# Kernel optimization log

Hardware: AMD Instinct MI355X
Metric: run time of the kernel (lower is better)

Reference implementation:

```python
import jax, jax.numpy as jnp
import numpy as np

N = 100000   # n_entity
D = 128      # kg_emb_dim
R = 12       # n_relation
NB = 8       # num_bases
E = 1_000_000
P = 400_000  # hypergraph incidences
HE = 20_000  # hyperedges
B = 64       # users in batch
LR = 64      # related entities per hypergraph per user
LC = 32      # context entities per user
NH = 8       # mha heads
HD = D // NH


def setup_inputs() -> dict:
    key = jax.random.key(0)
    ks = jax.random.split(key, 32)
    s = 1.0 / np.sqrt(D)
    f = lambda i, shape, sc=s: jax.random.normal(ks[i], shape, dtype=jnp.float32) * sc
    ri = lambda i, shape, hi: jax.random.randint(ks[i], shape, 0, hi, dtype=jnp.int32)
    return {
        'entity_emb': f(0, (N, D)),
        'rgcn_bases': f(1, (NB, D, D)),
        'rgcn_comp': f(2, (R, NB)),
        'rgcn_root': f(3, (D, D)),
        'rgcn_bias': jnp.zeros((D,), jnp.float32),
        'sess_theta': f(4, (D, D)),
        'sess_bias': jnp.zeros((D,), jnp.float32),
        'know_theta': f(5, (D, D)),
        'know_bias': jnp.zeros((D,), jnp.float32),
        'in_proj_w': f(6, (3 * D, D)),
        'in_proj_b': jnp.zeros((3 * D,), jnp.float32),
        'out_proj_w': f(7, (D, D)),
        'out_proj_b': jnp.zeros((D,), jnp.float32),
        'attn_his_a': f(8, (D, D)),
        'attn_his_b': f(9, (D, 1)),
        'attn_a': f(10, (D, D)),
        'attn_b': f(11, (D, 1)),
        'rec_bias': jnp.zeros((N,), jnp.float32),
        'edge_src': ri(12, (E,), N),
        'edge_dst': ri(13, (E,), N),
        'edge_type': ri(14, (E,), R),
        'sess_nodes': ri(15, (P,), N),
        'sess_edges': ri(16, (P,), HE),
        'know_nodes': ri(17, (P,), N),
        'know_edges': ri(18, (P,), HE),
        'sess_rel_idx': ri(19, (B, LR), N),
        'know_rel_idx': ri(20, (B, LR), N),
        'context_idx': ri(21, (B, LC), N),
    }


def rgcn_conv(x, bases, comp, root, bias, src, dst, etype):
    # PyG RGCNConv with basis decomposition; per-relation mean aggregation
    # norm = 1/|N_r(i)| : count edges per (dst, relation)
    pair_key = dst * R + etype
    cnt = jax.ops.segment_sum(jnp.ones_like(src, dtype=x.dtype), pair_key, N * R)
    norm = 1.0 / jnp.maximum(cnt[pair_key], 1.0)  # [E]
    w = jnp.einsum('rb,bio->rio', comp, bases)    # [R, D, D]
    out = x @ root + bias
    for r in range(R):
        h_r = x @ w[r]                                            # [N, D]
        coef = norm * (etype == r).astype(x.dtype)                # [E]
        out = out + jax.ops.segment_sum(h_r[src] * coef[:, None], dst, N)
    return out


def hypergraph_conv(x, theta, bias, nodes, edges, n_hyperedges):
    # PyG HypergraphConv (no attention): D^-1 H W B^-1 H^T X Theta + bias
    xt = x @ theta                                                # [N, D]
    ones = jnp.ones(nodes.shape, x.dtype)
    b_deg = jax.ops.segment_sum(ones, edges, n_hyperedges)        # [HE]
    edge_feat = jax.ops.segment_sum(xt[nodes], edges, n_hyperedges)
    edge_feat = edge_feat * jnp.where(b_deg > 0, 1.0 / b_deg, 0.0)[:, None]
    d_deg = jax.ops.segment_sum(ones, nodes, N)                   # [N]
    out = jax.ops.segment_sum(edge_feat[edges], nodes, N)
    return out * jnp.where(d_deg > 0, 1.0 / d_deg, 0.0)[:, None] + bias


def self_attn_batch(h, a, b):
    # SelfAttentionBatch: e = tanh(h a) b; softmax over nodes; weighted sum
    e = jnp.einsum('bld,dk->blk', jnp.tanh(jnp.einsum('bld,de->ble', h, a)), b)[..., 0]
    attn = jax.nn.softmax(e, axis=-1)                             # [B, L]
    return jnp.einsum('bl,bld->bd', attn, h)


def mha(q, kv, in_proj_w, in_proj_b, out_proj_w, out_proj_b):
    # torch.nn.MultiheadAttention (batch_first) math
    wq, wk, wv = in_proj_w[:D], in_proj_w[D:2 * D], in_proj_w[2 * D:]
    bq, bk, bv = in_proj_b[:D], in_proj_b[D:2 * D], in_proj_b[2 * D:]
    qh = (q @ wq.T + bq).reshape(q.shape[0], q.shape[1], NH, HD)
    kh = (kv @ wk.T + bk).reshape(kv.shape[0], kv.shape[1], NH, HD)
    vh = (kv @ wv.T + bv).reshape(kv.shape[0], kv.shape[1], NH, HD)
    logits = jnp.einsum('bqhd,bkhd->bhqk', qh, kh) / np.sqrt(HD)
    attn = jax.nn.softmax(logits, axis=-1)
    o = jnp.einsum('bhqk,bkhd->bqhd', attn, vh).reshape(q.shape[0], q.shape[1], D)
    return o @ out_proj_w.T + out_proj_b


def reference(entity_emb, rgcn_bases, rgcn_comp, rgcn_root, rgcn_bias,
              sess_theta, sess_bias, know_theta, know_bias,
              in_proj_w, in_proj_b, out_proj_w, out_proj_b,
              attn_his_a, attn_his_b, attn_a, attn_b, rec_bias,
              edge_src, edge_dst, edge_type,
              sess_nodes, sess_edges, know_nodes, know_edges,
              sess_rel_idx, know_rel_idx, context_idx):
    # 1) RGCN over the full KG
    kg = rgcn_conv(entity_emb, rgcn_bases, rgcn_comp, rgcn_root, rgcn_bias,
                   edge_src, edge_dst, edge_type)
    # 2) session / knowledge hypergraph convolutions on RGCN output
    sess = hypergraph_conv(kg, sess_theta, sess_bias, sess_nodes, sess_edges, HE)
    know = hypergraph_conv(kg, know_theta, know_bias, know_nodes, know_edges, HE)
    # 3) per-user: related = concat(session_emb, knowledge_emb); context from kg
    related = jnp.concatenate([sess[sess_rel_idx], know[know_rel_idx]], axis=1)  # [B, 2LR, D]
    context = kg[context_idx]                                                    # [B, LC, D]
    # 4) MHItemAttention (context queries related) + gated attention pooling
    att_rel = mha(context, related, in_proj_w, in_proj_b, out_proj_w, out_proj_b)
    his = self_attn_batch(att_rel, attn_his_a, attn_his_b)                       # [B, D]
    user_cat = jnp.concatenate([context, his[:, None, :]], axis=1)               # [B, LC+1, D]
    user = self_attn_batch(user_cat, attn_a, attn_b)                             # [B, D]
    # 5) recommendation scores: F.linear(user, kg_embedding, rec_bias.bias)
    return user @ kg.T + rec_bias                                                # [B, N]
```

## Files before the change

### kernel.cpp

```cpp
#include <hip/hip_runtime.h>
#include <hip/hip_bf16.h>

#define DN 100000
#define DD 128
#define DR 12
#define DNB 8
#define DE 1000000
#define DP 400000
#define DHE 20000
#define DHE2 40000
#define DB 64
#define DLR 64
#define DLC 32
#define DNH 8
#define DHD 16
#define NRBINS (DR * DN)
#define NALLBINS (NRBINS + DHE2)
#define SCAN_CHUNK 1024
#define MCAP 65536

typedef unsigned short ushortT;
typedef unsigned int uintT;
typedef __attribute__((ext_vector_type(8))) short s8v;
typedef __attribute__((ext_vector_type(4))) float f4v;

#define APAD 136
#define ASLB 40

__device__ __forceinline__ ushortT rneb(float v) {
    uintT b = __float_as_uint(v);
    return (ushortT)((b + 0x7FFFu + ((b >> 16) & 1u)) >> 16);
}
__device__ __forceinline__ float b2f(ushortT h) {
    return __uint_as_float(((uintT)h) << 16);
}

__device__ __forceinline__ void split_store8(ushortT* hbase, ushortT* lbase, const float* v)
{
    ushortT h[8], l[8];
    #pragma unroll
    for (int j = 0; j < 8; ++j) {
        h[j] = rneb(v[j]);
        l[j] = rneb(v[j] - b2f(h[j]));
    }
    uint4 hv = make_uint4((uintT)h[0] | ((uintT)h[1] << 16), (uintT)h[2] | ((uintT)h[3] << 16),
                          (uintT)h[4] | ((uintT)h[5] << 16), (uintT)h[6] | ((uintT)h[7] << 16));
    uint4 lv = make_uint4((uintT)l[0] | ((uintT)l[1] << 16), (uintT)l[2] | ((uintT)l[3] << 16),
                          (uintT)l[4] | ((uintT)l[5] << 16), (uintT)l[6] | ((uintT)l[7] << 16));
    *(uint4*)hbase = hv;
    *(uint4*)lbase = lv;
}

__global__ __launch_bounds__(256) void k_presplit_all(
    const float* __restrict__ root, const float* __restrict__ st,
    const float* __restrict__ kt, const float* __restrict__ ipw,
    const float* __restrict__ opw, const float* __restrict__ aha,
    const float* __restrict__ aa, ushortT* __restrict__ outA)
{
    int gid = blockIdx.x * 256 + threadIdx.x;
    int mat = gid >> 14, e = gid & 16383;
    const float* srcs[9] = {root, st, kt, ipw, ipw + 16384, ipw + 32768, opw, aha, aa};
    const float* W = srcs[mat];
    bool t1 = (mat >= 3 && mat <= 6);
    int k = e & 31, n = (e >> 5) & 127, kc = e >> 12;
    float f = t1 ? W[(size_t)n * 128 + kc * 32 + k] : W[(size_t)(kc * 32 + k) * 128 + n];
    ushortT h = rneb(f);
    outA[(size_t)mat * 32768 + e] = h;
    outA[(size_t)mat * 32768 + 16384 + e] = rneb(f - b2f(h));
}

__global__ void k_wcomp_split(const float* __restrict__ comp, const float* __restrict__ bases,
                              ushortT* __restrict__ warena)
{
    int i = blockIdx.x * blockDim.x + threadIdx.x;
    if (i >= DR * DD * DD) return;
    int r = i / (DD * DD), io = i % (DD * DD);
    float s = 0.f;
    #pragma unroll
    for (int b = 0; b < DNB; ++b) s += comp[r * DNB + b] * bases[(size_t)b * DD * DD + io];
    int irow = io >> 7, o = io & 127;
    int kc = irow >> 5, k = irow & 31;
    size_t dst = (size_t)r * 32768 + (size_t)kc * 4096 + o * 32 + k;
    ushortT h = rneb(s);
    warena[dst] = h;
    warena[dst + 16384] = rneb(s - b2f(h));
}

__global__ __launch_bounds__(256) void k_gemm_ds(
    const float* __restrict__ A, const ushortT* __restrict__ Wb,
    const float* __restrict__ bias, const float* __restrict__ rs,
    const int* __restrict__ gidx, float* __restrict__ gout,
    float* __restrict__ C, int M)
{
    __shared__ __align__(16) ushortT Ah[64 * APAD], Al[64 * APAD];
    __shared__ __align__(16) ushortT Bs[8192];
    int tid = threadIdx.x;
    int row0 = blockIdx.x * 64;
    {
        int row = tid >> 2, c0 = (tid & 3) * 32;
        int gr = row0 + row;
        int arow = gr;
        if (gidx && gr < M) arow = gidx[gr];
        const float* ar = A + (size_t)arow * 128 + c0;
        float sc = 1.0f;
        if (rs && gr < M) { float d = rs[gr]; sc = (d > 0.f) ? 1.0f / d : 0.f; }
        #pragma unroll
        for (int g = 0; g < 4; ++g) {
            float v[8] = {};
            if (gr < M) {
                float4 u0 = *(const float4*)(ar + g * 8);
                float4 u1 = *(const float4*)(ar + g * 8 + 4);
                v[0]=u0.x*sc; v[1]=u0.y*sc; v[2]=u0.z*sc; v[3]=u0.w*sc;
                v[4]=u1.x*sc; v[5]=u1.y*sc; v[6]=u1.z*sc; v[7]=u1.w*sc;
                if (gout) {
                    *(float4*)(gout + (size_t)gr * 128 + c0 + g * 8)     = u0;
                    *(float4*)(gout + (size_t)gr * 128 + c0 + g * 8 + 4) = u1;
                }
            }
            split_store8(&Ah[row * APAD + c0 + g * 8], &Al[row * APAD + c0 + g * 8], v);
        }
    }
    f4v acc[8] = {};
    int w = tid >> 6, lane = tid & 63, m = lane & 15, quad = lane >> 4;
    for (int kc = 0; kc < 4; ++kc) {
        __syncthreads();
        {
            const ushortT* gh = Wb + kc * 4096;
            const ushortT* gl = Wb + 16384 + kc * 4096;
            *(s8v*)&Bs[tid * 8]        = *(const s8v*)&gh[tid * 8];
            *(s8v*)&Bs[2048 + tid * 8] = *(const s8v*)&gh[2048 + tid * 8];
            *(s8v*)&Bs[4096 + tid * 8] = *(const s8v*)&gl[tid * 8];
            *(s8v*)&Bs[6144 + tid * 8] = *(const s8v*)&gl[2048 + tid * 8];
        }
        __syncthreads();
        s8v ah = *(const s8v*)&Ah[(w * 16 + m) * APAD + kc * 32 + quad * 8];
        s8v al = *(const s8v*)&Al[(w * 16 + m) * APAD + kc * 32 + quad * 8];
        #pragma unroll
        for (int nt = 0; nt < 8; ++nt) {
            int boff = (nt * 16 + m) * 32 + quad * 8;
            s8v bh = *(const s8v*)&Bs[boff];
            s8v bl = *(const s8v*)&Bs[4096 + boff];
            acc[nt] = __builtin_amdgcn_mfma_f32_16x16x32_bf16(ah, bh, acc[nt], 0, 0, 0);
            acc[nt] = __builtin_amdgcn_mfma_f32_16x16x32_bf16(al, bh, acc[nt], 0, 0, 0);
            acc[nt] = __builtin_amdgcn_mfma_f32_16x16x32_bf16(ah, bl, acc[nt], 0, 0, 0);
        }
    }
    float bv[8];
    #pragma unroll
    for (int nt = 0; nt < 8; ++nt) bv[nt] = bias ? bias[nt * 16 + m] : 0.f;
    #pragma unroll
    for (int rr = 0; rr < 4; ++rr) {
        int gr = row0 + w * 16 + quad * 4 + rr;
        if (gr < M) {
            #pragma unroll
            for (int nt = 0; nt < 8; ++nt)
                C[(size_t)gr * 128 + nt * 16 + m] = acc[nt][rr] + bv[nt];
        }
    }
}

__global__ __launch_bounds__(256) void k_tanh_dot_ds(
    const float* __restrict__ A, const ushortT* __restrict__ Wb,
    const float* __restrict__ bvec, float* __restrict__ e, int M)
{
    __shared__ __align__(16) ushortT Ah[64 * APAD], Al[64 * APAD];
    __shared__ __align__(16) ushortT Bs[8192];
    int tid = threadIdx.x;
    int row0 = blockIdx.x * 64;
    {
        int row = tid >> 2, c0 = (tid & 3) * 32;
        int gr = row0 + row;
        const float* ar = A + (size_t)gr * 128 + c0;
        #pragma unroll
        for (int g = 0; g < 4; ++g) {
            float v[8] = {};
            if (gr < M) {
                float4 u0 = *(const float4*)(ar + g * 8);
                float4 u1 = *(const float4*)(ar + g * 8 + 4);
                v[0]=u0.x; v[1]=u0.y; v[2]=u0.z; v[3]=u0.w;
                v[4]=u1.x; v[5]=u1.y; v[6]=u1.z; v[7]=u1.w;
            }
            split_store8(&Ah[row * APAD + c0 + g * 8], &Al[row * APAD + c0 + g * 8], v);
        }
    }
    f4v acc[8] = {};
    int w = tid >> 6, lane = tid & 63, m = lane & 15, quad = lane >> 4;
    for (int kc = 0; kc < 4; ++kc) {
        __syncthreads();
        {
            const ushortT* gh = Wb + kc * 4096;
            const ushortT* gl = Wb + 16384 + kc * 4096;
            *(s8v*)&Bs[tid * 8]        = *(const s8v*)&gh[tid * 8];
            *(s8v*)&Bs[2048 + tid * 8] = *(const s8v*)&gh[2048 + tid * 8];
            *(s8v*)&Bs[4096 + tid * 8] = *(const s8v*)&gl[tid * 8];
            *(s8v*)&Bs[6144 + tid * 8] = *(const s8v*)&gl[2048 + tid * 8];
        }
        __syncthreads();
        s8v ah = *(const s8v*)&Ah[(w * 16 + m) * APAD + kc * 32 + quad * 8];
        s8v al = *(const s8v*)&Al[(w * 16 + m) * APAD + kc * 32 + quad * 8];
        #pragma unroll
        for (int nt = 0; nt < 8; ++nt) {
            int boff = (nt * 16 + m) * 32 + quad * 8;
            s8v bh = *(const s8v*)&Bs[boff];
            s8v bl = *(const s8v*)&Bs[4096 + boff];
            acc[nt] = __builtin_amdgcn_mfma_f32_16x16x32_bf16(ah, bh, acc[nt], 0, 0, 0);
            acc[nt] = __builtin_amdgcn_mfma_f32_16x16x32_bf16(al, bh, acc[nt], 0, 0, 0);
            acc[nt] = __builtin_amdgcn_mfma_f32_16x16x32_bf16(ah, bl, acc[nt], 0, 0, 0);
        }
    }
    float bv[8];
    #pragma unroll
    for (int nt = 0; nt < 8; ++nt) bv[nt] = bvec[nt * 16 + m];
    #pragma unroll
    for (int rr = 0; rr < 4; ++rr) {
        float p = 0.f;
        #pragma unroll
        for (int nt = 0; nt < 8; ++nt) p += tanhf(acc[nt][rr]) * bv[nt];
        #pragma unroll
        for (int o = 1; o < 16; o <<= 1) p += __shfl_xor(p, o);
        int gr = row0 + w * 16 + quad * 4 + rr;
        if (m == 0 && gr < M) e[gr] = p;
    }
}

template <int L>
__global__ __launch_bounds__(128) void k_pool_apply(const float* __restrict__ h,
                                                    const float* __restrict__ e,
                                                    float* __restrict__ out,
                                                    ushortT* __restrict__ us)
{
    __shared__ float es[L];
    int b = blockIdx.x, tid = threadIdx.x;
    if (tid < L) es[tid] = e[b * L + tid];
    __syncthreads();
    float mx = -1e30f;
    #pragma unroll
    for (int l = 0; l < L; ++l) mx = fmaxf(mx, es[l]);
    float wgt[L];
    float sum = 0.f;
    #pragma unroll
    for (int l = 0; l < L; ++l) { wgt[l] = __expf(es[l] - mx); sum += wgt[l]; }
    float inv = 1.0f / sum;
    float o = 0.f;
    #pragma unroll
    for (int l = 0; l < L; ++l) o += wgt[l] * h[((size_t)b * L + l) * 128 + tid];
    float val = o * inv;
    out[(size_t)b * 128 + tid] = val;
    if (us) {
        ushortT hh = rneb(val);
        ushortT ll = rneb(val - b2f(hh));
        int e_ = ((tid >> 5) * 2048) + b * 32 + (tid & 31);
        us[e_] = hh;
        us[8192 + e_] = ll;
    }
}

__global__ void k_build_ucat(const float* __restrict__ ctx, const float* __restrict__ his,
                             float* ucat)
{
    int i = blockIdx.x * blockDim.x + threadIdx.x;
    if (i >= DB * 33 * 128) return;
    int d = i & 127, l = (i >> 7) % 33, b = i / (33 * 128);
    ucat[i] = (l < 32) ? ctx[((size_t)b * 32 + l) * 128 + d] : his[(size_t)b * 128 + d];
}

__global__ __launch_bounds__(256) void k_rgcn_fk(
    const float* __restrict__ x, const ushortT* __restrict__ rootsplit,
    const ushortT* __restrict__ warena, const float* __restrict__ bias,
    const int* __restrict__ soff, const int* __restrict__ hist,
    const int* __restrict__ ssrc, float* __restrict__ kg)
{
    __shared__ __align__(16) ushortT Ah[64 * ASLB], Al[64 * ASLB];
    __shared__ __align__(16) ushortT Bs[8192];
    int tid = threadIdx.x;
    int dst0 = blockIdx.x * 64;
    int nrow = min(64, DN - dst0);
    int w = tid >> 6, lane = tid & 63, m = lane & 15, quad = lane >> 4;
    int row = tid >> 2, ci = (tid & 3) * 8;
    f4v acc[8] = {};

    for (int s = 0; s < 52; ++s) {
        int r = (s - 4) >> 2, kci = (s - 4) & 3;
        __syncthreads();
        {
            float a[8] = {};
            if (row < nrow) {
                if (s < 4) {
                    const float* ar = x + (size_t)(dst0 + row) * 128 + s * 32 + ci;
                    float4 u0 = *(const float4*)ar, u1 = *(const float4*)(ar + 4);
                    a[0]=u0.x; a[1]=u0.y; a[2]=u0.z; a[3]=u0.w;
                    a[4]=u1.x; a[5]=u1.y; a[6]=u1.z; a[7]=u1.w;
                } else {
                    int key = (dst0 + row) * DR + r;
                    int len = hist[key];
                    int st = soff[key] - len;
                    int cb = kci * 32 + ci;
                    for (int i = 0; i < len; ++i) {
                        const float* xr = x + (size_t)ssrc[st + i] * 128 + cb;
                        float4 v0 = *(const float4*)xr, v1 = *(const float4*)(xr + 4);
                        a[0]+=v0.x; a[1]+=v0.y; a[2]+=v0.z; a[3]+=v0.w;
                        a[4]+=v1.x; a[5]+=v1.y; a[6]+=v1.z; a[7]+=v1.w;
                    }
                    float inv = (len > 0) ? 1.0f / (float)len : 0.f;
                    #pragma unroll
                    for (int j = 0; j < 8; ++j) a[j] *= inv;
                }
            }
            split_store8(&Ah[row * ASLB + ci], &Al[row * ASLB + ci], a);
        }
        {
            const ushortT* bb = (s < 4) ? rootsplit + s * 4096
                                        : warena + (size_t)r * 32768 + kci * 4096;
            const ushortT* bl = (s < 4) ? rootsplit + 16384 + s * 4096
                                        : warena + (size_t)r * 32768 + 16384 + kci * 4096;
            *(s8v*)&Bs[tid * 8]        = *(const s8v*)&bb[tid * 8];
            *(s8v*)&Bs[2048 + tid * 8] = *(const s8v*)&bb[2048 + tid * 8];
            *(s8v*)&Bs[4096 + tid * 8] = *(const s8v*)&bl[tid * 8];
            *(s8v*)&Bs[6144 + tid * 8] = *(const s8v*)&bl[2048 + tid * 8];
        }
        __syncthreads();
        s8v ah = *(const s8v*)&Ah[(w * 16 + m) * ASLB + quad * 8];
        s8v al = *(const s8v*)&Al[(w * 16 + m) * ASLB + quad * 8];
        #pragma unroll
        for (int nt = 0; nt < 8; ++nt) {
            int boff = (nt * 16 + m) * 32 + quad * 8;
            s8v bh = *(const s8v*)&Bs[boff];
            s8v bl2 = *(const s8v*)&Bs[4096 + boff];
            acc[nt] = __builtin_amdgcn_mfma_f32_16x16x32_bf16(ah, bh, acc[nt], 0, 0, 0);
            acc[nt] = __builtin_amdgcn_mfma_f32_16x16x32_bf16(al, bh, acc[nt], 0, 0, 0);
            acc[nt] = __builtin_amdgcn_mfma_f32_16x16x32_bf16(ah, bl2, acc[nt], 0, 0, 0);
        }
    }
    float bv[8];
    #pragma unroll
    for (int nt = 0; nt < 8; ++nt) bv[nt] = bias[nt * 16 + m];
    #pragma unroll
    for (int rr = 0; rr < 4; ++rr) {
        int gr = dst0 + w * 16 + quad * 4 + rr;
        if (gr < DN) {
            #pragma unroll
            for (int nt = 0; nt < 8; ++nt)
                kg[(size_t)gr * 128 + nt * 16 + m] = acc[nt][rr] + bv[nt];
        }
    }
}

__global__ __launch_bounds__(256) void k_score_ds(
    const float* __restrict__ kg, const ushortT* __restrict__ Ub,
    const float* __restrict__ rb, float* __restrict__ out)
{
    __shared__ __align__(16) ushortT Ah[64 * APAD], Al[64 * APAD];
    __shared__ __align__(16) ushortT Bs[4096];
    int tid = threadIdx.x;
    int n0 = blockIdx.x * 64;
    {
        int row = tid >> 2, c0 = (tid & 3) * 32;
        int gr = n0 + row;
        const float* ar = kg + (size_t)gr * 128 + c0;
        #pragma unroll
        for (int g = 0; g < 4; ++g) {
            float v[8] = {};
            if (gr < DN) {
                float4 u0 = *(const float4*)(ar + g * 8);
                float4 u1 = *(const float4*)(ar + g * 8 + 4);
                v[0]=u0.x; v[1]=u0.y; v[2]=u0.z; v[3]=u0.w;
                v[4]=u1.x; v[5]=u1.y; v[6]=u1.z; v[7]=u1.w;
            }
            split_store8(&Ah[row * APAD + c0 + g * 8], &Al[row * APAD + c0 + g * 8], v);
        }
    }
    f4v acc[4] = {};
    int w = tid >> 6, lane = tid & 63, m = lane & 15, quad = lane >> 4;
    for (int kc = 0; kc < 4; ++kc) {
        __syncthreads();
        {
            const ushortT* gh = Ub + kc * 2048;
            const ushortT* gl = Ub + 8192 + kc * 2048;
            *(s8v*)&Bs[tid * 8]        = *(const s8v*)&gh[tid * 8];
            *(s8v*)&Bs[2048 + tid * 8] = *(const s8v*)&gl[tid * 8];
        }
        __syncthreads();
        s8v ah = *(const s8v*)&Ah[(w * 16 + m) * APAD + kc * 32 + quad * 8];
        s8v al = *(const s8v*)&Al[(w * 16 + m) * APAD + kc * 32 + quad * 8];
        #pragma unroll
        for (int nt = 0; nt < 4; ++nt) {
            int boff = (nt * 16 + m) * 32 + quad * 8;
            s8v bh = *(const s8v*)&Bs[boff];
            s8v bl = *(const s8v*)&Bs[2048 + boff];
            acc[nt] = __builtin_amdgcn_mfma_f32_16x16x32_bf16(ah, bh, acc[nt], 0, 0, 0);
            acc[nt] = __builtin_amdgcn_mfma_f32_16x16x32_bf16(al, bh, acc[nt], 0, 0, 0);
            acc[nt] = __builtin_amdgcn_mfma_f32_16x16x32_bf16(ah, bl, acc[nt], 0, 0, 0);
        }
    }
    int n = n0 + w * 16 + quad * 4;
    if (n < DN) {
        float4 rbv = *(const float4*)&rb[n];
        #pragma unroll
        for (int nt = 0; nt < 4; ++nt) {
            int b = nt * 16 + m;
            float4 o = make_float4(acc[nt][0] + rbv.x, acc[nt][1] + rbv.y,
                                   acc[nt][2] + rbv.z, acc[nt][3] + rbv.w);
            *(float4*)&out[(size_t)b * DN + n] = o;
        }
    }
}

__global__ void k_scan_pass1(const int* __restrict__ in, int n, int* __restrict__ bsum)
{
    __shared__ int red[256];
    int b = blockIdx.x, t = threadIdx.x;
    int i0 = b * SCAN_CHUNK + t * 4;
    int s = 0;
    #pragma unroll
    for (int j = 0; j < 4; ++j) {
        int i = i0 + j;
        if (i < n) s += in[i];
    }
    red[t] = s;
    __syncthreads();
    for (int o = 128; o > 0; o >>= 1) {
        if (t < o) red[t] += red[t + o];
        __syncthreads();
    }
    if (t == 0) bsum[b] = red[0];
}

__global__ __launch_bounds__(256) void k_scan_pass2p(int* bsum, int nb, int* total)
{
    __shared__ int lds[256];
    __shared__ int carry;
    int t = threadIdx.x;
    if (t == 0) carry = 0;
    __syncthreads();
    for (int c0 = 0; c0 < nb; c0 += 256) {
        int i = c0 + t;
        int v = (i < nb) ? bsum[i] : 0;
        lds[t] = v;
        __syncthreads();
        for (int o = 1; o < 256; o <<= 1) {
            int add = (t >= o) ? lds[t - o] : 0;
            __syncthreads();
            lds[t] += add;
            __syncthreads();
        }
        int myc = carry;
        if (i < nb) bsum[i] = lds[t] - v + myc;
        int tot = lds[255];
        __syncthreads();
        if (t == 0) carry = myc + tot;
        __syncthreads();
    }
    if (total && t == 0) *total = carry;
}

__global__ void k_scan_pass3(const int* __restrict__ in, int n, const int* __restrict__ bsum,
                             int* __restrict__ out)
{
    __shared__ int lds[256];
    int b = blockIdx.x, t = threadIdx.x;
    int i0 = b * SCAN_CHUNK + t * 4;
    int v[4]; int s = 0;
    #pragma unroll
    for (int j = 0; j < 4; ++j) {
        int i = i0 + j;
        int x = 0;
        if (i < n) x = in[i];
        v[j] = x; s += x;
    }
    lds[t] = s;
    __syncthreads();
    for (int o = 1; o < 256; o <<= 1) {
        int add = (t >= o) ? lds[t - o] : 0;
        __syncthreads();
        lds[t] += add;
        __syncthreads();
    }
    int run = lds[t] - s + bsum[b];
    #pragma unroll
    for (int j = 0; j < 4; ++j) {
        int i = i0 + j;
        if (i < n) { out[i] = run; run += v[j]; }
    }
}

__global__ void k_hist_both(const int* __restrict__ dst, const int* __restrict__ et,
                            int* __restrict__ hist,
                            const int* __restrict__ se, const int* __restrict__ ke)
{
    int i = blockIdx.x * blockDim.x + threadIdx.x;
    if (i < DE) {
        atomicAdd(&hist[dst[i] * DR + et[i]], 1);
    } else {
        int j = i - DE;
        if (j < DP) atomicAdd(&hist[NRBINS + se[j]], 1);
        else if (j < 2 * DP) atomicAdd(&hist[NRBINS + DHE + ke[j - DP]], 1);
    }
}

__global__ void k_bucket_both(const int* __restrict__ src, const int* __restrict__ dst,
                              const int* __restrict__ et, int* __restrict__ soff,
                              int* __restrict__ ssrc,
                              const int* __restrict__ sn, const int* __restrict__ se,
                              const int* __restrict__ kn, const int* __restrict__ ke,
                              int* __restrict__ pns)
{
    int i = blockIdx.x * blockDim.x + threadIdx.x;
    if (i < DE) {
        int key = dst[i] * DR + et[i];
        int pos = atomicAdd(&soff[key], 1);
        ssrc[pos] = src[i];
    } else {
        int j = i - DE;
        if (j >= 2 * DP) return;
        int e, node;
        if (j < DP) { e = se[j]; node = sn[j]; }
        else { e = DHE + ke[j - DP]; node = kn[j - DP]; }
        int pos = atomicAdd(&soff[NRBINS + e], 1);
        pns[pos - DE] = node;
    }
}

__global__ void k_hyper_agg(const float* __restrict__ xsrc, const int* __restrict__ pns,
                            const int* __restrict__ hoff, const int* __restrict__ hcnt,
                            const int* __restrict__ heneed, float* __restrict__ efeat)
{
    int lane = threadIdx.x & 63;
    int he = (blockIdx.x * blockDim.x + threadIdx.x) >> 6;
    if (he >= DHE2) return;
    if (!heneed[he]) return;
    int len = hcnt[he];
    int st = hoff[he] - len - DE;
    int half = lane >> 5;
    int c16 = (lane & 31) * 4;
    float4 acc = make_float4(0.f, 0.f, 0.f, 0.f);
    int c = 0;
    for (; c + 4 <= len; c += 4) {
        int n0 = pns[st + c + half];
        int n1 = pns[st + c + 2 + half];
        float4 v0 = *(const float4*)&xsrc[(size_t)n0 * 128 + c16];
        float4 v1 = *(const float4*)&xsrc[(size_t)n1 * 128 + c16];
        acc.x += v0.x + v1.x; acc.y += v0.y + v1.y;
        acc.z += v0.z + v1.z; acc.w += v0.w + v1.w;
    }
    for (; c < len; c += 2) {
        int idx = c + half;
        if (idx < len) {
            int n = pns[st + idx];
            float4 v = *(const float4*)&xsrc[(size_t)n * 128 + c16];
            acc.x += v.x; acc.y += v.y; acc.z += v.z; acc.w += v.w;
        }
    }
    acc.x += __shfl_xor(acc.x, 32);
    acc.y += __shfl_xor(acc.y, 32);
    acc.z += __shfl_xor(acc.z, 32);
    acc.w += __shfl_xor(acc.w, 32);
    if (half == 0) {
        float inv = (len > 0) ? 1.0f / (float)len : 0.f;
        float4 o = make_float4(acc.x * inv, acc.y * inv, acc.z * inv, acc.w * inv);
        *(float4*)&efeat[(size_t)he * 128 + c16] = o;
    }
}

__global__ void k_slot_assign2(const int* __restrict__ sidx, const int* __restrict__ kidx,
                               int* slot_s, int* slot_k, int* scnt)
{
    int i = blockIdx.x * blockDim.x + threadIdx.x;
    if (i < DB * DLR) {
        int node = sidx[i];
        if (atomicCAS(&slot_s[node], -1, -2) == -1) slot_s[node] = atomicAdd(&scnt[0], 1);
    } else if (i < 2 * DB * DLR) {
        int node = kidx[i - DB * DLR];
        if (atomicCAS(&slot_k[node], -1, -2) == -1) slot_k[node] = atomicAdd(&scnt[1], 1);
    }
}

__global__ __launch_bounds__(256) void k_sdeg_match(
    const int* __restrict__ nodes, const int* __restrict__ he, const int* __restrict__ slot,
    float* sdeg, int* mcnt, int* mhe, int* msl, int* heneed, int heBase)
{
    __shared__ int lcnt, lbase;
    if (threadIdx.x == 0) lcnt = 0;
    __syncthreads();
    int i = blockIdx.x * 256 + threadIdx.x;
    int s = -1, lidx = 0, h = 0;
    if (i < DP) {
        s = slot[nodes[i]];
        if (s >= 0) {
            h = heBase + he[i];
            heneed[h] = 1;
            atomicAdd(&sdeg[s], 1.0f);
            lidx = atomicAdd(&lcnt, 1);
        }
    }
    __syncthreads();
    if (threadIdx.x == 0) lbase = (lcnt > 0) ? atomicAdd(mcnt, lcnt) : 0;
    __syncthreads();
    if (s >= 0) {
        int idx = lbase + lidx;
        if (idx < MCAP) { mhe[idx] = h; msl[idx] = s; }
    }
}

__global__ void k_accmatch2(const float* __restrict__ efeat,
                            const int* __restrict__ mhe_s, const int* __restrict__ msl_s,
                            const int* __restrict__ mhe_k, const int* __restrict__ msl_k,
                            const int* __restrict__ mcnt,
                            float* sacc_s, float* sacc_k)
{
    int lane = threadIdx.x & 63;
    int w = (blockIdx.x * blockDim.x + threadIdx.x) >> 6;
    int nw = (gridDim.x * blockDim.x) >> 6;
    int Ms = min(mcnt[0], MCAP), Mk = min(mcnt[1], MCAP);
    for (int i = w; i < Ms + Mk; i += nw) {
        bool sess = i < Ms;
        int he = sess ? mhe_s[i] : mhe_k[i - Ms];
        int sl = sess ? msl_s[i] : msl_k[i - Ms];
        float* sacc = sess ? sacc_s : sacc_k;
        float2 v = *(const float2*)&efeat[(size_t)he * 128 + lane * 2];
        atomicAdd(&sacc[(size_t)sl * 128 + lane * 2],     v.x);
        atomicAdd(&sacc[(size_t)sl * 128 + lane * 2 + 1], v.y);
    }
}

__global__ void k_rel_gather2(const float* __restrict__ so_s, const float* __restrict__ so_k,
                              const int* __restrict__ slot_s, const int* __restrict__ slot_k,
                              const int* __restrict__ ridx_s, const int* __restrict__ ridx_k,
                              float* __restrict__ related)
{
    int gid = blockIdx.x * blockDim.x + threadIdx.x;
    int i = gid >> 5, c = gid & 31;
    if (i >= 2 * DB * DLR) return;
    bool sess = i < DB * DLR;
    int ii = sess ? i : i - DB * DLR;
    int s = sess ? slot_s[ridx_s[ii]] : slot_k[ridx_k[ii]];
    const float* so = sess ? so_s : so_k;
    int b = ii / DLR, l = ii % DLR;
    int colOff = sess ? 0 : 64;
    ((float4*)&related[((size_t)b * 128 + colOff + l) * 128])[c] =
        ((const float4*)&so[(size_t)s * 128])[c];
}

__global__ __launch_bounds__(256) void k_mha(const float* __restrict__ qb,
                                             const float* __restrict__ kb,
                                             const float* __restrict__ vb,
                                             float* __restrict__ ob)
{
    int b = blockIdx.x >> 3, h = blockIdx.x & 7;
    __shared__ float Ks[128][16], Vs[128][16], Qs[32][16];
    int tid = threadIdx.x;
    for (int i = tid; i < 128 * 16; i += 256) {
        int j = i >> 4, d = i & 15;
        Ks[j][d] = kb[((size_t)b * 128 + j) * 128 + h * 16 + d];
        Vs[j][d] = vb[((size_t)b * 128 + j) * 128 + h * 16 + d];
    }
    for (int i = tid; i < 32 * 16; i += 256) {
        int q = i >> 4, d = i & 15;
        Qs[q][d] = qb[((size_t)b * 32 + q) * 128 + h * 16 + d] * 0.25f;
    }
    __syncthreads();
    int q = tid >> 3;
    int jg = tid & 7;
    float lg[16];
    float m = -1e30f;
    #pragma unroll
    for (int jj = 0; jj < 16; ++jj) {
        int j = jg * 16 + jj;
        float s = 0.f;
        #pragma unroll
        for (int d = 0; d < 16; ++d) s += Qs[q][d] * Ks[j][d];
        lg[jj] = s;
        m = fmaxf(m, s);
    }
    #pragma unroll
    for (int o = 1; o < 8; o <<= 1) m = fmaxf(m, __shfl_xor(m, o));
    float sum = 0.f;
    float acc[16] = {};
    #pragma unroll
    for (int jj = 0; jj < 16; ++jj) {
        float p = __expf(lg[jj] - m);
        sum += p;
        int j = jg * 16 + jj;
        #pragma unroll
        for (int d = 0; d < 16; ++d) acc[d] += p * Vs[j][d];
    }
    #pragma unroll
    for (int o = 1; o < 8; o <<= 1) {
        sum += __shfl_xor(sum, o);
        #pragma unroll
        for (int d = 0; d < 16; ++d) acc[d] += __shfl_xor(acc[d], o);
    }
    if (jg == 0) {
        float inv = 1.0f / sum;
        #pragma unroll
        for (int d = 0; d < 16; ++d)
            ob[((size_t)b * 32 + q) * 128 + h * 16 + d] = acc[d] * inv;
    }
}

extern "C" void kernel_launch(void* const* d_in, const int* in_sizes, int n_in,
                              void* d_out, int out_size, void* d_ws, size_t ws_size,
                              hipStream_t stream)
{
    const float* emb        = (const float*)d_in[0];
    const float* bases      = (const float*)d_in[1];
    const float* comp       = (const float*)d_in[2];
    const float* root       = (const float*)d_in[3];
    const float* rgcn_bias  = (const float*)d_in[4];
    const float* sess_theta = (const float*)d_in[5];
    const float* sess_bias  = (const float*)d_in[6];
    const float* know_theta = (const float*)d_in[7];
    const float* know_bias  = (const float*)d_in[8];
    const float* in_proj_w  = (const float*)d_in[9];
    const float* in_proj_b  = (const float*)d_in[10];
    const float* out_proj_w = (const float*)d_in[11];
    const float* out_proj_b = (const float*)d_in[12];
    const float* attn_his_a = (const float*)d_in[13];
    const float* attn_his_b = (const float*)d_in[14];
    const float* attn_a     = (const float*)d_in[15];
    const float* attn_b     = (const float*)d_in[16];
    const float* rec_bias   = (const float*)d_in[17];
    const int* edge_src     = (const int*)d_in[18];
    const int* edge_dst     = (const int*)d_in[19];
    const int* edge_type    = (const int*)d_in[20];
    const int* sess_nodes   = (const int*)d_in[21];
    const int* sess_edges   = (const int*)d_in[22];
    const int* know_nodes   = (const int*)d_in[23];
    const int* know_edges   = (const int*)d_in[24];
    const int* sess_rel_idx = (const int*)d_in[25];
    const int* know_rel_idx = (const int*)d_in[26];
    const int* context_idx  = (const int*)d_in[27];
    float* out = (float*)d_out;

    float* wsf = (float*)d_ws;
    size_t off = 0;
    auto alloc = [&](size_t n) { size_t r = off; off += (n + 255) & ~(size_t)255; return r; };
    float* kg      = wsf + alloc(12800000);
    float* tmp     = wsf + alloc(12800000);
    ushortT* warena = (ushortT*)(wsf + alloc(196608));
    int*   bsumV   = (int*)(wsf + alloc(2048));
    size_t zstart = off;
    int*   heneed  = (int*)(wsf + alloc(DHE2));
    int*   mcnt    = (int*)(wsf + alloc(16));
    int*   scnt    = (int*)(wsf + alloc(16));
    float* sdeg_s  = wsf + alloc(4096);
    float* sdeg_k  = wsf + alloc(4096);
    float* sacc_s  = wsf + alloc(524288);
    float* sacc_k  = wsf + alloc(524288);
    size_t zend = off;
    size_t fstart = off;
    int*   slot_s  = (int*)(wsf + alloc(100000));
    int*   slot_k  = (int*)(wsf + alloc(100000));
    size_t fend = off;
    int*   pns     = (int*)(wsf + alloc(2 * DP));
    int*   mhe_s   = (int*)(wsf + alloc(MCAP));
    int*   msl_s   = (int*)(wsf + alloc(MCAP));
    int*   mhe_k   = (int*)(wsf + alloc(MCAP));
    int*   msl_k   = (int*)(wsf + alloc(MCAP));
    float* so_s    = wsf + alloc(524288);
    float* so_k    = wsf + alloc(524288);
    float* related = wsf + alloc(1048576);
    float* ctx     = wsf + alloc(262144);
    float* qb      = wsf + alloc(262144);
    float* kb      = wsf + alloc(1048576);
    float* vb      = wsf + alloc(1048576);
    float* obuf    = wsf + alloc(262144);
    float* attrel  = wsf + alloc(262144);
    float* his     = wsf + alloc(8192);
    float* ucat    = wsf + alloc(270336);
    float* userb   = wsf + alloc(8192);
    float* e1      = wsf + alloc(2048);
    float* e2      = wsf + alloc(2112);
    (void)ws_size; (void)in_sizes; (void)n_in; (void)out_size;

    int*   hist    = (int*)tmp;
    int*   soff    = (int*)tmp + 1240000;
    int*   ssrc    = (int*)tmp + 2480000;
    float* efeat   = tmp + 3600000;
    ushortT* wsplit = (ushortT*)(tmp + 12200000);
    ushortT* usplit = (ushortT*)(tmp + 12400000);

    const int nbA = (NALLBINS + SCAN_CHUNK - 1) / SCAN_CHUNK;

    hipMemsetAsync(wsf + zstart, 0, (zend - zstart) * 4, stream);
    hipMemsetAsync(wsf + fstart, 0xFF, (fend - fstart) * 4, stream);
    hipMemsetAsync(hist, 0, (size_t)NALLBINS * 4, stream);

    k_presplit_all<<<576, 256, 0, stream>>>(root, sess_theta, know_theta, in_proj_w,
                                            out_proj_w, attn_his_a, attn_a, wsplit);

    k_slot_assign2<<<32, 256, 0, stream>>>(sess_rel_idx, know_rel_idx, slot_s, slot_k, scnt);
    k_sdeg_match<<<(DP + 255) / 256, 256, 0, stream>>>(sess_nodes, sess_edges, slot_s,
                                                       sdeg_s, mcnt, mhe_s, msl_s, heneed, 0);
    k_sdeg_match<<<(DP + 255) / 256, 256, 0, stream>>>(know_nodes, know_edges, slot_k,
                                                       sdeg_k, mcnt + 1, mhe_k, msl_k, heneed, DHE);

    k_hist_both<<<(DE + 2 * DP + 255) / 256, 256, 0, stream>>>(edge_dst, edge_type, hist,
                                                               sess_edges, know_edges);
    k_scan_pass1<<<nbA, 256, 0, stream>>>(hist, NALLBINS, bsumV);
    k_scan_pass2p<<<1, 256, 0, stream>>>(bsumV, nbA, nullptr);
    k_scan_pass3<<<nbA, 256, 0, stream>>>(hist, NALLBINS, bsumV, soff);
    k_bucket_both<<<(DE + 2 * DP + 255) / 256, 256, 0, stream>>>(
        edge_src, edge_dst, edge_type, soff, ssrc,
        sess_nodes, sess_edges, know_nodes, know_edges, pns);

    k_wcomp_split<<<(DR * DD * DD + 255) / 256, 256, 0, stream>>>(comp, bases, warena);

    int gemmN = (DN + 63) / 64;
    k_rgcn_fk<<<gemmN, 256, 0, stream>>>(emb, wsplit + 0 * 32768, warena, rgcn_bias,
                                         soff, hist, ssrc, kg);

    k_hyper_agg<<<(DHE2 * 64 + 255) / 256, 256, 0, stream>>>(kg, pns, soff + NRBINS,
                                                             hist + NRBINS, heneed, efeat);
    k_accmatch2<<<256, 256, 0, stream>>>(efeat, mhe_s, msl_s, mhe_k, msl_k, mcnt, sacc_s, sacc_k);

    k_gemm_ds<<<64, 256, 0, stream>>>(sacc_s, wsplit + 1 * 32768, sess_bias, sdeg_s,
                                      nullptr, nullptr, so_s, 4096);
    k_gemm_ds<<<64, 256, 0, stream>>>(sacc_k, wsplit + 2 * 32768, know_bias, sdeg_k,
                                      nullptr, nullptr, so_k, 4096);
    k_rel_gather2<<<(2 * DB * DLR * 32 + 255) / 256, 256, 0, stream>>>(
        so_s, so_k, slot_s, slot_k, sess_rel_idx, know_rel_idx, related);

    k_gemm_ds<<<(DB * DLC + 63) / 64, 256, 0, stream>>>(kg, wsplit + 3 * 32768,
                                                        in_proj_b, nullptr,
                                                        context_idx, ctx, qb, DB * DLC);
    k_gemm_ds<<<(DB * 128 + 63) / 64, 256, 0, stream>>>(related, wsplit + 4 * 32768,
                                                        in_proj_b + DD, nullptr,
                                                        nullptr, nullptr, kb, DB * 128);
    k_gemm_ds<<<(DB * 128 + 63) / 64, 256, 0, stream>>>(related, wsplit + 5 * 32768,
                                                        in_proj_b + 2 * DD, nullptr,
                                                        nullptr, nullptr, vb, DB * 128);
    k_mha<<<DB * DNH, 256, 0, stream>>>(qb, kb, vb, obuf);
    k_gemm_ds<<<(DB * DLC + 63) / 64, 256, 0, stream>>>(obuf, wsplit + 6 * 32768,
                                                        out_proj_b, nullptr,
                                                        nullptr, nullptr, attrel, DB * DLC);

    k_tanh_dot_ds<<<(DB * DLC + 63) / 64, 256, 0, stream>>>(attrel, wsplit + 7 * 32768,
                                                            attn_his_b, e1, DB * DLC);
    k_pool_apply<32><<<DB, 128, 0, stream>>>(attrel, e1, his, nullptr);
    k_build_ucat<<<(DB * 33 * 128 + 255) / 256, 256, 0, stream>>>(ctx, his, ucat);
    k_tanh_dot_ds<<<(DB * 33 + 63) / 64, 256, 0, stream>>>(ucat, wsplit + 8 * 32768,
                                                           attn_b, e2, DB * 33);
    k_pool_apply<33><<<DB, 128, 0, stream>>>(ucat, e2, userb, usplit);
    k_score_ds<<<gemmN, 256, 0, stream>>>(kg, usplit, rec_bias, out);
}
```

Measured before the change: 943.3 us.

## Gather full neighbor rows once per relation and pad B tile in LDS

The fused RGCN kernel now gathers all 128 columns of each neighbor row in one pass per relation, keeping 32 floats per thread in registers. Previously it walked the neighbor list four times, once per 32-column chunk. This cuts repeated index loads and scattered row reads to a quarter. The weight tile in shared memory is re-laid out with a padded row stride (40) to avoid LDS bank conflicts on the MFMA B-operand reads. The trade-off is more registers per thread, which may lower occupancy.

```diff
diff --git a/kernel.cpp b/kernel.cpp
--- a/kernel.cpp
+++ b/kernel.cpp
@@ -26,6 +26,7 @@
 
 #define APAD 136
 #define ASLB 40
+#define BSP 40
 
 __device__ __forceinline__ ushortT rneb(float v) {
     uintT b = __float_as_uint(v);
@@ -271,64 +272,76 @@
     const int* __restrict__ ssrc, float* __restrict__ kg)
 {
     __shared__ __align__(16) ushortT Ah[64 * ASLB], Al[64 * ASLB];
-    __shared__ __align__(16) ushortT Bs[8192];
+    __shared__ __align__(16) ushortT Bs[2 * 128 * BSP];
     int tid = threadIdx.x;
     int dst0 = blockIdx.x * 64;
     int nrow = min(64, DN - dst0);
     int w = tid >> 6, lane = tid & 63, m = lane & 15, quad = lane >> 4;
     int row = tid >> 2, ci = (tid & 3) * 8;
+    int brow = tid & 127, bpl = tid >> 7;
     f4v acc[8] = {};
 
-    for (int s = 0; s < 52; ++s) {
-        int r = (s - 4) >> 2, kci = (s - 4) & 3;
-        __syncthreads();
-        {
-            float a[8] = {};
-            if (row < nrow) {
-                if (s < 4) {
-                    const float* ar = x + (size_t)(dst0 + row) * 128 + s * 32 + ci;
-                    float4 u0 = *(const float4*)ar, u1 = *(const float4*)(ar + 4);
-                    a[0]=u0.x; a[1]=u0.y; a[2]=u0.z; a[3]=u0.w;
-                    a[4]=u1.x; a[5]=u1.y; a[6]=u1.z; a[7]=u1.w;
-                } else {
-                    int key = (dst0 + row) * DR + r;
-                    int len = hist[key];
-                    int st = soff[key] - len;
-                    int cb = kci * 32 + ci;
-                    for (int i = 0; i < len; ++i) {
-                        const float* xr = x + (size_t)ssrc[st + i] * 128 + cb;
-                        float4 v0 = *(const float4*)xr, v1 = *(const float4*)(xr + 4);
-                        a[0]+=v0.x; a[1]+=v0.y; a[2]+=v0.z; a[3]+=v0.w;
-                        a[4]+=v1.x; a[5]+=v1.y; a[6]+=v1.z; a[7]+=v1.w;
+    for (int p = 0; p < 13; ++p) {
+        float a[32];
+        if (row < nrow) {
+            if (p == 0) {
+                const float* ar = x + (size_t)(dst0 + row) * 128 + ci;
+                #pragma unroll
+                for (int k = 0; k < 4; ++k) {
+                    float4 u0 = *(const float4*)(ar + k * 32);
+                    float4 u1 = *(const float4*)(ar + k * 32 + 4);
+                    a[k*8+0]=u0.x; a[k*8+1]=u0.y; a[k*8+2]=u0.z; a[k*8+3]=u0.w;
+                    a[k*8+4]=u1.x; a[k*8+5]=u1.y; a[k*8+6]=u1.z; a[k*8+7]=u1.w;
+                }
+            } else {
+                #pragma unroll
+                for (int j = 0; j < 32; ++j) a[j] = 0.f;
+                int key = (dst0 + row) * DR + (p - 1);
+                int len = hist[key];
+                int st = soff[key] - len;
+                for (int i = 0; i < len; ++i) {
+                    const float* xr = x + (size_t)ssrc[st + i] * 128 + ci;
+                    #pragma unroll
+                    for (int k = 0; k < 4; ++k) {
+                        float4 u0 = *(const float4*)(xr + k * 32);
+                        float4 u1 = *(const float4*)(xr + k * 32 + 4);
+                        a[k*8+0]+=u0.x; a[k*8+1]+=u0.y; a[k*8+2]+=u0.z; a[k*8+3]+=u0.w;
+                        a[k*8+4]+=u1.x; a[k*8+5]+=u1.y; a[k*8+6]+=u1.z; a[k*8+7]+=u1.w;
                     }
-                    float inv = (len > 0) ? 1.0f / (float)len : 0.f;
-                    #pragma unroll
-                    for (int j = 0; j < 8; ++j) a[j] *= inv;
                 }
+                float inv = (len > 0) ? 1.0f / (float)len : 0.f;
+                #pragma unroll
+                for (int j = 0; j < 32; ++j) a[j] *= inv;
             }
-            split_store8(&Ah[row * ASLB + ci], &Al[row * ASLB + ci], a);
-        }
-        {
-            const ushortT* bb = (s < 4) ? rootsplit + s * 4096
-                                        : warena + (size_t)r * 32768 + kci * 4096;
-            const ushortT* bl = (s < 4) ? rootsplit + 16384 + s * 4096
-                                        : warena + (size_t)r * 32768 + 16384 + kci * 4096;
-            *(s8v*)&Bs[tid * 8]        = *(const s8v*)&bb[tid * 8];
-            *(s8v*)&Bs[2048 + tid * 8] = *(const s8v*)&bb[2048 + tid * 8];
-            *(s8v*)&Bs[4096 + tid * 8] = *(const s8v*)&bl[tid * 8];
-            *(s8v*)&Bs[6144 + tid * 8] = *(const s8v*)&bl[2048 + tid * 8];
-        }
-        __syncthreads();
-        s8v ah = *(const s8v*)&Ah[(w * 16 + m) * ASLB + quad * 8];
-        s8v al = *(const s8v*)&Al[(w * 16 + m) * ASLB + quad * 8];
-        #pragma unroll
-        for (int nt = 0; nt < 8; ++nt) {
-            int boff = (nt * 16 + m) * 32 + quad * 8;
-            s8v bh = *(const s8v*)&Bs[boff];
-            s8v bl2 = *(const s8v*)&Bs[4096 + boff];
-            acc[nt] = __builtin_amdgcn_mfma_f32_16x16x32_bf16(ah, bh, acc[nt], 0, 0, 0);
-            acc[nt] = __builtin_amdgcn_mfma_f32_16x16x32_bf16(al, bh, acc[nt], 0, 0, 0);
-            acc[nt] = __builtin_amdgcn_mfma_f32_16x16x32_bf16(ah, bl2, acc[nt], 0, 0, 0);
+        } else {
+            #pragma unroll
+            for (int j = 0; j < 32; ++j) a[j] = 0.f;
+        }
+        const ushortT* Wb = (p == 0) ? rootsplit : warena + (size_t)(p - 1) * 32768;
+        #pragma unroll
+        for (int kci = 0; kci < 4; ++kci) {
+            __syncthreads();
+            split_store8(&Ah[row * ASLB + ci], &Al[row * ASLB + ci], a + kci * 8);
+            {
+                const ushortT* src = Wb + bpl * 16384 + kci * 4096 + brow * 32;
+                ushortT* dstp = &Bs[bpl * (128 * BSP) + brow * BSP];
+                *(s8v*)&dstp[0]  = *(const s8v*)&src[0];
+                *(s8v*)&dstp[8]  = *(const s8v*)&src[8];
+                *(s8v*)&dstp[16] = *(const s8v*)&src[16];
+                *(s8v*)&dstp[24] = *(const s8v*)&src[24];
+            }
+            __syncthreads();
+            s8v ah = *(const s8v*)&Ah[(w * 16 + m) * ASLB + quad * 8];
+            s8v al = *(const s8v*)&Al[(w * 16 + m) * ASLB + quad * 8];
+            #pragma unroll
+            for (int nt = 0; nt < 8; ++nt) {
+                int boff = (nt * 16 + m) * BSP + quad * 8;
+                s8v bh = *(const s8v*)&Bs[boff];
+                s8v bl2 = *(const s8v*)&Bs[128 * BSP + boff];
+                acc[nt] = __builtin_amdgcn_mfma_f32_16x16x32_bf16(ah, bh, acc[nt], 0, 0, 0);
+                acc[nt] = __builtin_amdgcn_mfma_f32_16x16x32_bf16(al, bh, acc[nt], 0, 0, 0);
+                acc[nt] = __builtin_amdgcn_mfma_f32_16x16x32_bf16(ah, bl2, acc[nt], 0, 0, 0);
+            }
         }
     }
     float bv[8];
```

Result: faster. 806.4 us (-14.5%).
